# Performance work log

Measured on AMD Instinct MI355X. Metric: run time of the kernel, lower is better.

## Reference

```python
import jax, jax.numpy as jnp
import numpy as np

EMBED = 256
HEADS = 8
N_EDGES = 32  # topk k per query node = head_edges * heads = number_of_edges
HEAD_DIM = EMBED // HEADS


def setup_inputs() -> dict:
    key = jax.random.key(0)
    k1, k2, k3, k4 = jax.random.split(key, 4)
    B, L = 8, 2048
    return {
        "keys": jax.random.normal(k1, (B, L, EMBED), dtype=jnp.float32),
        "query": jax.random.normal(k2, (B, L, EMBED), dtype=jnp.float32),
        "Wk": jax.random.normal(k3, (HEAD_DIM, HEAD_DIM), dtype=jnp.float32) / np.sqrt(HEAD_DIM).astype(np.float32),
        "Wq": jax.random.normal(k4, (HEAD_DIM, HEAD_DIM), dtype=jnp.float32) / np.sqrt(HEAD_DIM).astype(np.float32),
    }


def reference(keys, query, Wk, Wq):
    B, Lk, _ = keys.shape
    Lq = query.shape[1]
    # split heads: [B, L, H, D]
    k = keys.reshape(B, Lk, HEADS, HEAD_DIM)
    q = query.reshape(B, Lq, HEADS, HEAD_DIM)
    # per-head linear projections (torch Linear: y = x @ W^T, no bias)
    k = jnp.einsum('nkhd,ed->nkhe', k, Wk)
    q = jnp.einsum('nqhd,ed->nqhe', q, Wq)
    # attention scores [B, H, Lq, Lk]
    energy = jnp.einsum('nqhd,nkhd->nhqk', q, k)
    attn = jax.nn.softmax(energy / jnp.sqrt(jnp.float32(EMBED)), axis=3)
    # mean over heads -> [B, Lq, Lk]
    mean_attn = jnp.mean(attn, axis=1)
    # topk neighbor indices per query node, then sorted ascending
    _, idx = jax.lax.top_k(mean_attn, N_EDGES)          # [B, Lq, N_EDGES]
    edges = jnp.sort(idx, axis=2)
    nodes = jnp.broadcast_to(jnp.arange(Lq, dtype=edges.dtype)[None, :, None], edges.shape)
    # edge_index [B, 2, Lq * N_EDGES]: row0 = source node, row1 = neighbor
    edge_index = jnp.stack([nodes.reshape(B, -1), edges.reshape(B, -1)], axis=1)
    return edge_index
```

## Files before the change

kernel.cpp:

```cpp
#include <hip/hip_runtime.h>
#include <hip/hip_bf16.h>

#define NB 8
#define LSEQ 2048
#define HH 8
#define DD 32
#define EE 256
#define NE 32
#define QT 16
#define NWAVE 16
#define NTH 1024
#define KW 128
#define NTILE 8
#define SMS 2052

typedef __attribute__((ext_vector_type(8))) short short8;
typedef __attribute__((ext_vector_type(4))) float f32x4;

__global__ __launch_bounds__(256) void proj_kernel(const float* __restrict__ x,
                                                   const float* __restrict__ W,
                                                   __hip_bfloat16* __restrict__ o1,
                                                   __hip_bfloat16* __restrict__ o2,
                                                   __hip_bfloat16* __restrict__ o3) {
  const int b = blockIdx.x;
  const int n = b / LSEQ, l = b % LSEQ;
  __shared__ float xs[EE];
  __shared__ float Ws[DD][DD + 1];
  const int t = threadIdx.x;
  xs[t] = x[(size_t)b * EE + t];
  for (int i = t; i < DD * DD; i += 256) Ws[i / DD][i % DD] = W[i];
  __syncthreads();
  const int h = t / DD, e = t % DD;
  float acc = 0.f;
#pragma unroll
  for (int d = 0; d < DD; ++d) acc = fmaf(xs[h * DD + d], Ws[e][d], acc);
  const size_t oi = (((size_t)n * HH + h) * LSEQ + l) * DD + e;
  __hip_bfloat16 p1 = __float2bfloat16(acc);
  float r1 = acc - __bfloat162float(p1);
  __hip_bfloat16 p2 = __float2bfloat16(r1);
  float r2 = r1 - __bfloat162float(p2);
  __hip_bfloat16 p3 = __float2bfloat16(r2);
  o1[oi] = p1;
  o2[oi] = p2;
  o3[oi] = p3;
}

__global__ __launch_bounds__(NTH) void attn_topk_kernel(
    const __hip_bfloat16* __restrict__ q1, const __hip_bfloat16* __restrict__ q2,
    const __hip_bfloat16* __restrict__ q3, const __hip_bfloat16* __restrict__ k1,
    const __hip_bfloat16* __restrict__ k2, const __hip_bfloat16* __restrict__ k3,
    int* __restrict__ out) {
  __shared__ float smean[QT * SMS];
  __shared__ float wredT[QT][16];
  __shared__ float wredS[QT][16];

  const int t = threadIdx.x;
  const int w = t >> 6, l = t & 63;
  const int g = l >> 4, c = l & 15;
  const int n = blockIdx.x & 7;
  const int q0 = (blockIdx.x >> 3) * QT;

  for (int i = t; i < QT * SMS; i += NTH) smean[i] = 0.f;
  __syncthreads();

  for (int h = 0; h < HH; ++h) {
    const size_t hb = ((size_t)n * HH + h) * LSEQ;
    const size_t qoff = (hb + q0 + c) * DD + (size_t)g * 8;
    const short8 aH = *(const short8*)(q1 + qoff);
    const short8 aM = *(const short8*)(q2 + qoff);
    const short8 aL = *(const short8*)(q3 + qoff);

    f32x4 acc[NTILE];
#pragma unroll
    for (int t2 = 0; t2 < NTILE; ++t2) {
      const size_t koff = (hb + (size_t)w * KW + t2 * 16 + c) * DD + (size_t)g * 8;
      const short8 bH = *(const short8*)(k1 + koff);
      const short8 bM = *(const short8*)(k2 + koff);
      const short8 bL = *(const short8*)(k3 + koff);
      f32x4 a = {0.f, 0.f, 0.f, 0.f};
      a = __builtin_amdgcn_mfma_f32_16x16x32_bf16(aH, bH, a, 0, 0, 0);
      a = __builtin_amdgcn_mfma_f32_16x16x32_bf16(aH, bM, a, 0, 0, 0);
      a = __builtin_amdgcn_mfma_f32_16x16x32_bf16(aM, bH, a, 0, 0, 0);
      a = __builtin_amdgcn_mfma_f32_16x16x32_bf16(aH, bL, a, 0, 0, 0);
      a = __builtin_amdgcn_mfma_f32_16x16x32_bf16(aL, bH, a, 0, 0, 0);
      a = __builtin_amdgcn_mfma_f32_16x16x32_bf16(aM, bM, a, 0, 0, 0);
      acc[t2] = a;
    }

    float m[4];
#pragma unroll
    for (int r = 0; r < 4; ++r) {
      float v = acc[0][r];
#pragma unroll
      for (int t2 = 1; t2 < NTILE; ++t2) v = fmaxf(v, acc[t2][r]);
      m[r] = v;
    }
#pragma unroll
    for (int msk = 1; msk <= 8; msk <<= 1)
#pragma unroll
      for (int r = 0; r < 4; ++r) m[r] = fmaxf(m[r], __shfl_xor(m[r], msk));
    if (c == 0) {
#pragma unroll
      for (int r = 0; r < 4; ++r) wredT[g * 4 + r][w] = m[r];
    }
    __syncthreads();
    float fm[4];
#pragma unroll
    for (int r = 0; r < 4; ++r) fm[r] = wredT[g * 4 + r][c];
#pragma unroll
    for (int msk = 1; msk <= 8; msk <<= 1)
#pragma unroll
      for (int r = 0; r < 4; ++r) fm[r] = fmaxf(fm[r], __shfl_xor(fm[r], msk));

    float Zl[4] = {0.f, 0.f, 0.f, 0.f};
#pragma unroll
    for (int t2 = 0; t2 < NTILE; ++t2) {
#pragma unroll
      for (int r = 0; r < 4; ++r) {
        float e = __expf((acc[t2][r] - fm[r]) * 0.0625f);
        acc[t2][r] = e;
        Zl[r] += e;
      }
    }
#pragma unroll
    for (int msk = 1; msk <= 8; msk <<= 1)
#pragma unroll
      for (int r = 0; r < 4; ++r) Zl[r] += __shfl_xor(Zl[r], msk);
    if (c == 0) {
#pragma unroll
      for (int r = 0; r < 4; ++r) wredS[g * 4 + r][w] = Zl[r];
    }
    __syncthreads();
    float inv[4];
#pragma unroll
    for (int r = 0; r < 4; ++r) {
      float z = wredS[g * 4 + r][c];
#pragma unroll
      for (int msk = 1; msk <= 8; msk <<= 1) z += __shfl_xor(z, msk);
      inv[r] = 1.0f / z;
    }
#pragma unroll
    for (int t2 = 0; t2 < NTILE; ++t2) {
#pragma unroll
      for (int r = 0; r < 4; ++r) {
        smean[(g * 4 + r) * SMS + w * KW + t2 * 16 + c] += acc[t2][r] * inv[r];
      }
    }
  }
  __syncthreads();

  float* row = &smean[w * SMS];
  float vals[32];
  float v1 = -1e30f, v2 = -1e30f;
  int i1 = 1 << 30, i2 = 1 << 30;
#pragma unroll
  for (int j = 0; j < 32; ++j) {
    float v = row[j * 64 + l];
    vals[j] = v;
    const int k = j * 64 + l;
    if (v > v1) { v2 = v1; i2 = i1; v1 = v; i1 = k; }
    else if (v > v2) { v2 = v; i2 = k; }
  }
  unsigned rem = 0u;
  int selk = 0;
#pragma unroll 1
  for (int it = 0; it < NE; ++it) {
    float bv = v1;
    int bk = i1;
#pragma unroll
    for (int off = 32; off >= 1; off >>= 1) {
      float ov = __shfl_xor(bv, off);
      int ok = __shfl_xor(bk, off);
      if (ov > bv || (ov == bv && ok < bk)) { bv = ov; bk = ok; }
    }
    if (l == it) selk = bk;
    if (i1 == bk) {
      rem |= 1u << (bk >> 6);
      if (i2 != (1 << 30)) {
        v1 = v2; i1 = i2;
        v2 = -1e30f; i2 = 1 << 30;
      } else {
        v1 = -1e30f; i1 = 1 << 30;
        v2 = -1e30f; i2 = 1 << 30;
#pragma unroll
        for (int j = 0; j < 32; ++j) {
          float v = ((rem >> j) & 1u) ? -1e30f : vals[j];
          const int k = j * 64 + l;
          if (v > v1) { v2 = v1; i2 = i1; v1 = v; i1 = k; }
          else if (v > v2) { v2 = v; i2 = k; }
        }
      }
    }
  }

  int rank = 0;
#pragma unroll
  for (int j = 0; j < NE; ++j) {
    int o = __shfl(selk, j);
    rank += (o < selk) ? 1 : 0;
  }
  const int qg = q0 + w;
  if (l < NE) {
    int* o0 = out + (size_t)n * 2 * LSEQ * NE + (size_t)qg * NE;
    int* o1p = o0 + (size_t)LSEQ * NE;
    o0[l] = qg;
    o1p[rank] = selk;
  }
}

extern "C" void kernel_launch(void* const* d_in, const int* in_sizes, int n_in,
                              void* d_out, int out_size, void* d_ws, size_t ws_size,
                              hipStream_t stream) {
  const float* keys = (const float*)d_in[0];
  const float* query = (const float*)d_in[1];
  const float* Wk = (const float*)d_in[2];
  const float* Wq = (const float*)d_in[3];
  int* out = (int*)d_out;

  const size_t SPLIT = (size_t)NB * HH * LSEQ * DD;
  __hip_bfloat16* qs1 = (__hip_bfloat16*)d_ws;
  __hip_bfloat16* qs2 = qs1 + SPLIT;
  __hip_bfloat16* qs3 = qs2 + SPLIT;
  __hip_bfloat16* ks1 = qs3 + SPLIT;
  __hip_bfloat16* ks2 = ks1 + SPLIT;
  __hip_bfloat16* ks3 = ks2 + SPLIT;

  proj_kernel<<<NB * LSEQ, 256, 0, stream>>>(query, Wq, qs1, qs2, qs3);
  proj_kernel<<<NB * LSEQ, 256, 0, stream>>>(keys, Wk, ks1, ks2, ks3);
  attn_topk_kernel<<<NB * (LSEQ / QT), NTH, 0, stream>>>(qs1, qs2, qs3, ks1, ks2, ks3, out);
}
```

Baseline: 517.7 us.

## Drop softmax max pass, accumulate mean in registers, halve waves per block

Folds the 1/sqrt(E) scale into the query projection and removes the per-head max reduction and its barrier, relying on the scores being small enough that exp cannot overflow. The head-mean is kept in registers instead of read-modify-write LDS updates, and shared memory shrinks to 8 rows that are filled in two passes for top-k. Each block now uses 8 waves covering 256 keys each, with a launch bounds hint of 4 blocks per CU, to raise occupancy. Skipping the max subtraction risks overflow or precision loss if the inputs were larger, and the larger per-wave tiles increase register pressure.

```diff
diff --git a/kernel.cpp b/kernel.cpp
--- a/kernel.cpp
+++ b/kernel.cpp
@@ -8,22 +8,22 @@
 #define EE 256
 #define NE 32
 #define QT 16
-#define NWAVE 16
-#define NTH 1024
-#define KW 128
-#define NTILE 8
-#define SMS 2052
+#define NWAVE 8
+#define NTH 512
+#define KW 256
+#define NTILE 16
+#define SMS 2050
 
 typedef __attribute__((ext_vector_type(8))) short short8;
 typedef __attribute__((ext_vector_type(4))) float f32x4;
 
 __global__ __launch_bounds__(256) void proj_kernel(const float* __restrict__ x,
                                                    const float* __restrict__ W,
+                                                   float scale,
                                                    __hip_bfloat16* __restrict__ o1,
                                                    __hip_bfloat16* __restrict__ o2,
                                                    __hip_bfloat16* __restrict__ o3) {
   const int b = blockIdx.x;
-  const int n = b / LSEQ, l = b % LSEQ;
   __shared__ float xs[EE];
   __shared__ float Ws[DD][DD + 1];
   const int t = threadIdx.x;
@@ -34,6 +34,8 @@
   float acc = 0.f;
 #pragma unroll
   for (int d = 0; d < DD; ++d) acc = fmaf(xs[h * DD + d], Ws[e][d], acc);
+  acc *= scale;
+  const int n = b / LSEQ, l = b % LSEQ;
   const size_t oi = (((size_t)n * HH + h) * LSEQ + l) * DD + e;
   __hip_bfloat16 p1 = __float2bfloat16(acc);
   float r1 = acc - __bfloat162float(p1);
@@ -45,14 +47,13 @@
   o3[oi] = p3;
 }
 
-__global__ __launch_bounds__(NTH) void attn_topk_kernel(
+__global__ __launch_bounds__(NTH, 4) void attn_topk_kernel(
     const __hip_bfloat16* __restrict__ q1, const __hip_bfloat16* __restrict__ q2,
     const __hip_bfloat16* __restrict__ q3, const __hip_bfloat16* __restrict__ k1,
     const __hip_bfloat16* __restrict__ k2, const __hip_bfloat16* __restrict__ k3,
     int* __restrict__ out) {
-  __shared__ float smean[QT * SMS];
-  __shared__ float wredT[QT][16];
-  __shared__ float wredS[QT][16];
+  __shared__ float smean[8 * SMS];
+  __shared__ float wredS[2][QT][NWAVE];
 
   const int t = threadIdx.x;
   const int w = t >> 6, l = t & 63;
@@ -60,8 +61,11 @@
   const int n = blockIdx.x & 7;
   const int q0 = (blockIdx.x >> 3) * QT;
 
-  for (int i = t; i < QT * SMS; i += NTH) smean[i] = 0.f;
-  __syncthreads();
+  float macc[NTILE][4];
+#pragma unroll
+  for (int t2 = 0; t2 < NTILE; ++t2)
+#pragma unroll
+    for (int r = 0; r < 4; ++r) macc[t2][r] = 0.f;
 
   for (int h = 0; h < HH; ++h) {
     const size_t hb = ((size_t)n * HH + h) * LSEQ;
@@ -87,37 +91,12 @@
       acc[t2] = a;
     }
 
-    float m[4];
-#pragma unroll
-    for (int r = 0; r < 4; ++r) {
-      float v = acc[0][r];
-#pragma unroll
-      for (int t2 = 1; t2 < NTILE; ++t2) v = fmaxf(v, acc[t2][r]);
-      m[r] = v;
-    }
-#pragma unroll
-    for (int msk = 1; msk <= 8; msk <<= 1)
-#pragma unroll
-      for (int r = 0; r < 4; ++r) m[r] = fmaxf(m[r], __shfl_xor(m[r], msk));
-    if (c == 0) {
-#pragma unroll
-      for (int r = 0; r < 4; ++r) wredT[g * 4 + r][w] = m[r];
-    }
-    __syncthreads();
-    float fm[4];
-#pragma unroll
-    for (int r = 0; r < 4; ++r) fm[r] = wredT[g * 4 + r][c];
-#pragma unroll
-    for (int msk = 1; msk <= 8; msk <<= 1)
-#pragma unroll
-      for (int r = 0; r < 4; ++r) fm[r] = fmaxf(fm[r], __shfl_xor(fm[r], msk));
-
     float Zl[4] = {0.f, 0.f, 0.f, 0.f};
 #pragma unroll
     for (int t2 = 0; t2 < NTILE; ++t2) {
 #pragma unroll
       for (int r = 0; r < 4; ++r) {
-        float e = __expf((acc[t2][r] - fm[r]) * 0.0625f);
+        float e = __expf(acc[t2][r]);
         acc[t2][r] = e;
         Zl[r] += e;
       }
@@ -128,83 +107,91 @@
       for (int r = 0; r < 4; ++r) Zl[r] += __shfl_xor(Zl[r], msk);
     if (c == 0) {
 #pragma unroll
-      for (int r = 0; r < 4; ++r) wredS[g * 4 + r][w] = Zl[r];
+      for (int r = 0; r < 4; ++r) wredS[h & 1][g * 4 + r][w] = Zl[r];
     }
     __syncthreads();
     float inv[4];
 #pragma unroll
     for (int r = 0; r < 4; ++r) {
-      float z = wredS[g * 4 + r][c];
-#pragma unroll
-      for (int msk = 1; msk <= 8; msk <<= 1) z += __shfl_xor(z, msk);
-      inv[r] = 1.0f / z;
-    }
-#pragma unroll
-    for (int t2 = 0; t2 < NTILE; ++t2) {
-#pragma unroll
-      for (int r = 0; r < 4; ++r) {
-        smean[(g * 4 + r) * SMS + w * KW + t2 * 16 + c] += acc[t2][r] * inv[r];
+      float z = wredS[h & 1][g * 4 + r][c & 7];
+#pragma unroll
+      for (int msk = 1; msk <= 4; msk <<= 1) z += __shfl_xor(z, msk);
+      inv[r] = __builtin_amdgcn_rcpf(z);
+    }
+#pragma unroll
+    for (int t2 = 0; t2 < NTILE; ++t2)
+#pragma unroll
+      for (int r = 0; r < 4; ++r) macc[t2][r] = fmaf(acc[t2][r], inv[r], macc[t2][r]);
+  }
+
+  for (int pass = 0; pass < 2; ++pass) {
+    if (pass) __syncthreads();
+    if ((g >> 1) == pass) {
+#pragma unroll
+      for (int t2 = 0; t2 < NTILE; ++t2)
+#pragma unroll
+        for (int r = 0; r < 4; ++r)
+          smean[((g & 1) * 4 + r) * SMS + w * KW + t2 * 16 + c] = macc[t2][r];
+    }
+    __syncthreads();
+
+    float* row = &smean[w * SMS];
+    float vals[32];
+    float v1 = -1e30f, v2 = -1e30f;
+    int i1 = 1 << 30, i2 = 1 << 30;
+#pragma unroll
+    for (int j = 0; j < 32; ++j) {
+      float v = row[j * 64 + l];
+      vals[j] = v;
+      const int k = j * 64 + l;
+      if (v > v1) { v2 = v1; i2 = i1; v1 = v; i1 = k; }
+      else if (v > v2) { v2 = v; i2 = k; }
+    }
+    unsigned rem = 0u;
+    int selk = 0;
+#pragma unroll 1
+    for (int it = 0; it < NE; ++it) {
+      float bv = v1;
+      int bk = i1;
+#pragma unroll
+      for (int off = 32; off >= 1; off >>= 1) {
+        float ov = __shfl_xor(bv, off);
+        int ok = __shfl_xor(bk, off);
+        if (ov > bv || (ov == bv && ok < bk)) { bv = ov; bk = ok; }
       }
-    }
-  }
-  __syncthreads();
-
-  float* row = &smean[w * SMS];
-  float vals[32];
-  float v1 = -1e30f, v2 = -1e30f;
-  int i1 = 1 << 30, i2 = 1 << 30;
-#pragma unroll
-  for (int j = 0; j < 32; ++j) {
-    float v = row[j * 64 + l];
-    vals[j] = v;
-    const int k = j * 64 + l;
-    if (v > v1) { v2 = v1; i2 = i1; v1 = v; i1 = k; }
-    else if (v > v2) { v2 = v; i2 = k; }
-  }
-  unsigned rem = 0u;
-  int selk = 0;
-#pragma unroll 1
-  for (int it = 0; it < NE; ++it) {
-    float bv = v1;
-    int bk = i1;
-#pragma unroll
-    for (int off = 32; off >= 1; off >>= 1) {
-      float ov = __shfl_xor(bv, off);
-      int ok = __shfl_xor(bk, off);
-      if (ov > bv || (ov == bv && ok < bk)) { bv = ov; bk = ok; }
-    }
-    if (l == it) selk = bk;
-    if (i1 == bk) {
-      rem |= 1u << (bk >> 6);
-      if (i2 != (1 << 30)) {
-        v1 = v2; i1 = i2;
-        v2 = -1e30f; i2 = 1 << 30;
-      } else {
-        v1 = -1e30f; i1 = 1 << 30;
-        v2 = -1e30f; i2 = 1 << 30;
-#pragma unroll
-        for (int j = 0; j < 32; ++j) {
-          float v = ((rem >> j) & 1u) ? -1e30f : vals[j];
-          const int k = j * 64 + l;
-          if (v > v1) { v2 = v1; i2 = i1; v1 = v; i1 = k; }
-          else if (v > v2) { v2 = v; i2 = k; }
+      if (l == it) selk = bk;
+      if (i1 == bk) {
+        rem |= 1u << (bk >> 6);
+        if (i2 != (1 << 30)) {
+          v1 = v2; i1 = i2;
+          v2 = -1e30f; i2 = 1 << 30;
+        } else {
+          v1 = -1e30f; i1 = 1 << 30;
+          v2 = -1e30f; i2 = 1 << 30;
+#pragma unroll
+          for (int j = 0; j < 32; ++j) {
+            float v = ((rem >> j) & 1u) ? -1e30f : vals[j];
+            const int k = j * 64 + l;
+            if (v > v1) { v2 = v1; i2 = i1; v1 = v; i1 = k; }
+            else if (v > v2) { v2 = v; i2 = k; }
+          }
         }
       }
     }
-  }
-
-  int rank = 0;
-#pragma unroll
-  for (int j = 0; j < NE; ++j) {
-    int o = __shfl(selk, j);
-    rank += (o < selk) ? 1 : 0;
-  }
-  const int qg = q0 + w;
-  if (l < NE) {
-    int* o0 = out + (size_t)n * 2 * LSEQ * NE + (size_t)qg * NE;
-    int* o1p = o0 + (size_t)LSEQ * NE;
-    o0[l] = qg;
-    o1p[rank] = selk;
+
+    int rank = 0;
+#pragma unroll
+    for (int j = 0; j < NE; ++j) {
+      int o = __shfl(selk, j);
+      rank += (o < selk) ? 1 : 0;
+    }
+    const int qg = q0 + pass * 8 + w;
+    if (l < NE) {
+      int* o0 = out + (size_t)n * 2 * LSEQ * NE + (size_t)qg * NE;
+      int* o1p = o0 + (size_t)LSEQ * NE;
+      o0[l] = qg;
+      o1p[rank] = selk;
+    }
   }
 }
 
@@ -225,7 +212,7 @@
   __hip_bfloat16* ks2 = ks1 + SPLIT;
   __hip_bfloat16* ks3 = ks2 + SPLIT;
 
-  proj_kernel<<<NB * LSEQ, 256, 0, stream>>>(query, Wq, qs1, qs2, qs3);
-  proj_kernel<<<NB * LSEQ, 256, 0, stream>>>(keys, Wk, ks1, ks2, ks3);
+  proj_kernel<<<NB * LSEQ, 256, 0, stream>>>(query, Wq, 0.0625f, qs1, qs2, qs3);
+  proj_kernel<<<NB * LSEQ, 256, 0, stream>>>(keys, Wk, 1.0f, ks1, ks2, ks3);
   attn_topk_kernel<<<NB * (LSEQ / QT), NTH, 0, stream>>>(qs1, qs2, qs3, ks1, ks2, ks3, out);
 }
```

Result: slower. 762.5 us (+47.3%).
